# Kernel optimization log

Hardware: AMD Instinct MI355X
Metric: run time of the kernel (lower is better)

Reference implementation:

```python
import jax, jax.numpy as jnp
import numpy as np
from math import sqrt

H = 16  # head_num


def setup_inputs() -> dict:
    key = jax.random.key(0)
    ks = jax.random.split(key, 8)
    B, Sq, Skv, Dq, Dkv, Dall = 2, 2048, 2048, 1024, 1024, 1024
    x = jax.random.normal(ks[0], (B, Sq, Dq), dtype=jnp.float32)
    y = jax.random.normal(ks[1], (B, Skv, Dkv), dtype=jnp.float32)
    attention_mask = jnp.ones((B, 1, Sq, Skv), dtype=jnp.int32)
    # torch nn.Linear weights are [out, in]
    Wq = jax.random.normal(ks[2], (Dall, Dq), dtype=jnp.float32) * 0.02
    Wk = jax.random.normal(ks[3], (Dall, Dkv), dtype=jnp.float32) * 0.02
    Wv = jax.random.normal(ks[4], (Dall, Dkv), dtype=jnp.float32) * 0.02
    Wo = jax.random.normal(ks[5], (Dq, Dall), dtype=jnp.float32) * 0.02
    bo = jnp.zeros((Dq,), dtype=jnp.float32)
    return {"x": x, "y": y, "attention_mask": attention_mask,
            "Wq": Wq, "Wk": Wk, "Wv": Wv, "Wo": Wo, "bo": bo}


def reference(x, y, attention_mask, Wq, Wk, Wv, Wo, bo):
    B, Sq, _ = x.shape
    Dall = Wq.shape[0]
    Dh = Dall // H
    # projections (torch Linear: x @ W.T), split heads -> [B, H, S, Dh]
    q = (x @ Wq.T).reshape(B, Sq, H, Dh).transpose(0, 2, 1, 3)
    k = (y @ Wk.T).reshape(B, -1, H, Dh).transpose(0, 2, 1, 3)
    v = (y @ Wv.T).reshape(B, -1, H, Dh).transpose(0, 2, 1, 3)
    scores = jnp.einsum('bhqd,bhkd->bhqk', q, k)  # [B,H,Sq,Skv]
    mask = (attention_mask == 0)  # masked_fill where mask.eq(0) -> but torch does mask.eq(0) then fills True positions
    scores = jnp.where(mask, jnp.float32(-1e9), scores)
    # NOTE: faithful quirk - mask applied before scaling; scale uses sqrt(h_size)
    attn = jax.nn.softmax(scores / sqrt(Dh), axis=-1)
    out = jnp.einsum('bhqk,bhkd->bhqd', attn, v)
    out = out.transpose(0, 2, 1, 3).reshape(B, Sq, Dall)
    return out @ Wo.T + bo
```

## Files before the change

kernel.cpp:

```cpp
#include <hip/hip_runtime.h>
#include <stdint.h>


typedef __attribute__((ext_vector_type(8))) short bf16x8;
typedef __attribute__((ext_vector_type(4))) float f32x4;
typedef __attribute__((ext_vector_type(16))) float f32x16;
typedef __attribute__((ext_vector_type(2))) unsigned int u32x2;

#define LOG2E 1.44269504088896f

static __device__ __forceinline__ unsigned short f2bf(float f) {
  union { float f; unsigned int u; } v; v.f = f;
  unsigned int r = v.u + 0x7FFFu + ((v.u >> 16) & 1u);
  return (unsigned short)(r >> 16);
}

static __device__ __forceinline__ void g2l16(const void* gsrc, void* ldst) {
  __builtin_amdgcn_global_load_lds((const __attribute__((address_space(1))) unsigned int*)gsrc,
                                   (__attribute__((address_space(3))) unsigned int*)ldst,
                                   16, 0, 0);
}

static __device__ __forceinline__ unsigned int cvt_pk_bf16(float lo, float hi) {
  unsigned int r;
  asm("v_cvt_pk_bf16_f32 %0, %1, %2" : "=v"(r) : "v"(lo), "v"(hi));
  return r;
}

static __device__ __forceinline__ u32x2 pl32swap(unsigned int a, unsigned int b) {
  return __builtin_amdgcn_permlane32_swap(a, b, false, false);
}

static __device__ __forceinline__ f32x16 mfma32(bf16x8 a, bf16x8 b, f32x16 c) {
  return __builtin_amdgcn_mfma_f32_32x32x16_bf16(a, b, c, 0, 0, 0);
}

static __device__ __forceinline__ size_t kfrag_addr(int row, int col) {
  int b = row >> 11, s = row & 2047;
  int h = col >> 6, d = col & 63;
  int t32 = s >> 5, r31 = s & 31;
  int ks = d >> 4, r5 = (d >> 3) & 1, e = d & 7;
  return (size_t)(b * 16 + h) * 131072 + (size_t)t32 * 2048 + ks * 512 + (r5 * 32 + r31) * 8 + e;
}
static __device__ __forceinline__ size_t vfrag_addr(int row, int col) {
  int b = row >> 11, s = row & 2047;
  int h = col >> 6, d = col & 63;
  int t64 = s >> 6, k2 = (s >> 4) & 3, r5 = (s >> 3) & 1, e = s & 7;
  int mb = d >> 5, r31 = d & 31;
  return (size_t)(b * 16 + h) * 131072 + (size_t)t64 * 4096 + (mb * 4 + k2) * 512 + (r5 * 32 + r31) * 8 + e;
}

__global__ void k_cvt2(const float* __restrict__ a, const float* __restrict__ b,
                       unsigned short* __restrict__ oa, unsigned short* __restrict__ ob, int n) {
  const float* in = blockIdx.y ? b : a;
  unsigned short* out = blockIdx.y ? ob : oa;
  int i = (blockIdx.x * blockDim.x + threadIdx.x) * 4;
  int stride = gridDim.x * blockDim.x * 4;
  for (; i < n; i += stride) {
    float4 v = *reinterpret_cast<const float4*>(in + i);
    ushort4 o;
    o.x = f2bf(v.x); o.y = f2bf(v.y); o.z = f2bf(v.z); o.w = f2bf(v.w);
    *reinterpret_cast<ushort4*>(out + i) = o;
  }
}

__global__ void k_cvt4(const float* __restrict__ a, const float* __restrict__ b,
                       const float* __restrict__ c, const float* __restrict__ d,
                       unsigned short* __restrict__ oa, unsigned short* __restrict__ ob,
                       unsigned short* __restrict__ oc, unsigned short* __restrict__ od, int n) {
  const float* in; unsigned short* out;
  switch (blockIdx.y) {
    case 0: in = a; out = oa; break;
    case 1: in = b; out = ob; break;
    case 2: in = c; out = oc; break;
    default: in = d; out = od; break;
  }
  int i = (blockIdx.x * blockDim.x + threadIdx.x) * 4;
  int stride = gridDim.x * blockDim.x * 4;
  for (; i < n; i += stride) {
    float4 v = *reinterpret_cast<const float4*>(in + i);
    ushort4 o;
    o.x = f2bf(v.x); o.y = f2bf(v.y); o.z = f2bf(v.z); o.w = f2bf(v.w);
    *reinterpret_cast<ushort4*>(out + i) = o;
  }
}

__global__ void k_pack_mask(const int* __restrict__ mask, unsigned long long* __restrict__ bits,
                            unsigned int* __restrict__ flag) {
  size_t gw = (size_t)blockIdx.x * 4 + (threadIdx.x >> 6);
  int lane = threadIdx.x & 63;
  int m = mask[gw * 64 + lane];
  unsigned long long bal = __ballot(m != 0);
  if (lane == 0) {
    bits[gw] = bal;
    if (bal != ~0ull) atomicAnd(flag, 0u);
  }
}

template <int OM>
static __device__ __forceinline__ void gemm_body(const unsigned short* __restrict__ A,
                                                 const unsigned short* __restrict__ W,
                                                 void* __restrict__ Cout,
                                                 const float* __restrict__ bias) {
  __shared__ __align__(16) unsigned short As[128 * 32];
  __shared__ __align__(16) unsigned short Bs[128 * 32];
  const int tid = threadIdx.x;
  const int w = tid >> 6, lane = tid & 63;
  const int wr = w >> 1, wc = w & 1;
  const int l15 = lane & 15, lg = lane >> 4;
  const int bm = blockIdx.x, bn = blockIdx.y;

  f32x4 acc[4][4] = {};

  const int e0 = w * 1024 + lane * 8;
  const int e1 = e0 + 512;
  const int r0 = e0 >> 5, c0 = e0 & 31;
  const int r1 = e1 >> 5, c1 = e1 & 31;
  const unsigned short* A0 = A + (size_t)(bm * 128 + r0) * 1024 + c0;
  const unsigned short* A1 = A + (size_t)(bm * 128 + r1) * 1024 + c1;
  const unsigned short* W0 = W + (size_t)(bn * 128 + r0) * 1024 + c0;
  const unsigned short* W1 = W + (size_t)(bn * 128 + r1) * 1024 + c1;

  for (int kt = 0; kt < 1024; kt += 32) {
    g2l16(A0 + kt, (char*)As + e0 * 2);
    g2l16(A1 + kt, (char*)As + e1 * 2);
    g2l16(W0 + kt, (char*)Bs + e0 * 2);
    g2l16(W1 + kt, (char*)Bs + e1 * 2);
    __syncthreads();
    bf16x8 a[4], b[4];
#pragma unroll
    for (int mi = 0; mi < 4; ++mi)
      a[mi] = *reinterpret_cast<const bf16x8*>(As + (wr * 64 + mi * 16 + l15) * 32 + lg * 8);
#pragma unroll
    for (int ni = 0; ni < 4; ++ni)
      b[ni] = *reinterpret_cast<const bf16x8*>(Bs + (wc * 64 + ni * 16 + l15) * 32 + lg * 8);
#pragma unroll
    for (int mi = 0; mi < 4; ++mi)
#pragma unroll
      for (int ni = 0; ni < 4; ++ni)
        acc[mi][ni] = __builtin_amdgcn_mfma_f32_16x16x32_bf16(a[mi], b[ni], acc[mi][ni], 0, 0, 0);
    __syncthreads();
  }

#pragma unroll
  for (int ni = 0; ni < 4; ++ni) {
    const int gcol = bn * 128 + wc * 64 + ni * 16 + l15;
    float bv = (OM == 1) ? bias[gcol] : 0.f;
#pragma unroll
    for (int mi = 0; mi < 4; ++mi) {
#pragma unroll
      for (int r = 0; r < 4; ++r) {
        const int grow = bm * 128 + wr * 64 + mi * 16 + lg * 4 + r;
        if (OM == 0)
          ((unsigned short*)Cout)[(size_t)grow * 1024 + gcol] = f2bf(acc[mi][ni][r]);
        else if (OM == 1)
          ((float*)Cout)[(size_t)grow * 1024 + gcol] = acc[mi][ni][r] + bv;
        else if (OM == 2)
          ((unsigned short*)Cout)[kfrag_addr(grow, gcol)] = f2bf(acc[mi][ni][r]);
        else
          ((unsigned short*)Cout)[vfrag_addr(grow, gcol)] = f2bf(acc[mi][ni][r]);
      }
    }
  }
}

__global__ __launch_bounds__(256) void k_gemm_qk(
    const unsigned short* __restrict__ xb, const unsigned short* __restrict__ yb,
    const unsigned short* __restrict__ Wq, const unsigned short* __restrict__ Wk,
    unsigned short* __restrict__ Qf, unsigned short* __restrict__ Kf) {
  const int z = blockIdx.z;
  gemm_body<2>(z ? yb : xb, z ? Wk : Wq, z ? Kf : Qf, nullptr);
}

__global__ __launch_bounds__(256) void k_gemm_v(
    const unsigned short* __restrict__ yb, const unsigned short* __restrict__ Wv,
    unsigned short* __restrict__ Vf) {
  gemm_body<3>(yb, Wv, Vf, nullptr);
}

__global__ __launch_bounds__(256) void k_gemm_o(
    const unsigned short* __restrict__ AO, const unsigned short* __restrict__ Wo,
    float* __restrict__ out, const float* __restrict__ bo) {
  gemm_body<1>(AO, Wo, out, bo);
}


#define BUILD_PB2(SP, K2, IDX) {                                   \
    unsigned int c0_ = cvt_pk_bf16(SP[(K2)*8 + 0], SP[(K2)*8 + 1]);\
    unsigned int c1_ = cvt_pk_bf16(SP[(K2)*8 + 2], SP[(K2)*8 + 3]);\
    unsigned int c2_ = cvt_pk_bf16(SP[(K2)*8 + 4], SP[(K2)*8 + 5]);\
    unsigned int c3_ = cvt_pk_bf16(SP[(K2)*8 + 6], SP[(K2)*8 + 7]);\
    u32x2 r0_ = pl32swap(c0_, c2_);                                \
    u32x2 r1_ = pl32swap(c1_, c3_);                                \
    union { unsigned int u[4]; bf16x8 v; } f_;                     \
    f_.u[0] = r0_.x; f_.u[1] = r1_.x; f_.u[2] = r0_.y; f_.u[3] = r1_.y; \
    pb[IDX] = f_.v; }

#define ATTN_STEP(c0, c1, n0, n1, T)                                          \
  {                                                                           \
    const int t_ = (T);                                                       \
    _Pragma("unroll")                                                         \
    for (int f = 0; f < 8; ++f)                                               \
      vf[f] = *reinterpret_cast<const bf16x8*>(Vbase + (size_t)t_ * 4096 + f * 512); \
    n0 = z16; n1 = z16;                                                       \
    _Pragma("unroll")                                                         \
    for (int ks = 0; ks < 4; ++ks) {                                          \
      n0 = mfma32(kf[ks], qf[ks], n0);                                        \
      n1 = mfma32(kf[4 + ks], qf[ks], n1);                                    \
    }                                                                         \
    const int t2_ = (t_ + 2) & 31;                                            \
    _Pragma("unroll")                                                         \
    for (int f = 0; f < 8; ++f)                                               \
      kf[f] = *reinterpret_cast<const bf16x8*>(Kbase + (size_t)t2_ * 4096 + f * 512); \
    if (!allfull) {                                                           \
      unsigned long long wb = brow[t_];                                       \
      if (!__all(wb == ~0ull)) {                                              \
        _Pragma("unroll")                                                     \
        for (int r = 0; r < 16; ++r) {                                        \
          const int kl = (r & 3) + 8 * (r >> 2) + 4 * hi;                     \
          c0[r] = ((wb >> kl) & 1ull) ? c0[r] : -1e9f;                        \
          c1[r] = ((wb >> (kl + 32)) & 1ull) ? c1[r] : -1e9f;                 \
        }                                                                     \
      }                                                                       \
    }                                                                         \
    float mx[8];                                                              \
    _Pragma("unroll")                                                         \
    for (int r = 0; r < 8; ++r)                                               \
      mx[r] = fmaxf(fmaxf(c0[r], c0[r + 8]), fmaxf(c1[r], c1[r + 8]));        \
    mx[0] = fmaxf(mx[0], mx[4]); mx[1] = fmaxf(mx[1], mx[5]);                 \
    mx[2] = fmaxf(mx[2], mx[6]); mx[3] = fmaxf(mx[3], mx[7]);                 \
    mx[0] = fmaxf(mx[0], mx[2]); mx[1] = fmaxf(mx[1], mx[3]);                 \
    float tm = fmaxf(mx[0], mx[1]);                                           \
    {                                                                         \
      u32x2 sw = pl32swap(__builtin_bit_cast(unsigned int, tm),               \
                          __builtin_bit_cast(unsigned int, tm));              \
      tm = fmaxf(__builtin_bit_cast(float, sw.x), __builtin_bit_cast(float, sw.y)); \
    }                                                                         \
    tm *= 0.125f;                                                             \
    if (__any(tm > m_run + 8.f)) {                                            \
      const float mn = fmaxf(m_run, tm);                                      \
      const float al = __builtin_amdgcn_exp2f((m_run - mn) * LOG2E);          \
      m_run = mn; l_run *= al;                                                \
      _Pragma("unroll")                                                       \
      for (int r = 0; r < 16; ++r) { o0[r] *= al; o1[r] *= al; }              \
    }                                                                         \
    const float mc_ = m_run * LOG2E;                                          \
    _Pragma("unroll")                                                         \
    for (int r = 0; r < 16; ++r) {                                            \
      c0[r] = __builtin_amdgcn_exp2f(c0[r] * C1 - mc_);                       \
      c1[r] = __builtin_amdgcn_exp2f(c1[r] * C1 - mc_);                       \
    }                                                                         \
    float sm[8];                                                              \
    _Pragma("unroll")                                                         \
    for (int r = 0; r < 8; ++r) sm[r] = (c0[r] + c0[r + 8]) + (c1[r] + c1[r + 8]); \
    sm[0] += sm[4]; sm[1] += sm[5]; sm[2] += sm[6]; sm[3] += sm[7];           \
    sm[0] += sm[2]; sm[1] += sm[3];                                           \
    float ls = sm[0] + sm[1];                                                 \
    {                                                                         \
      u32x2 sw = pl32swap(__builtin_bit_cast(unsigned int, ls),               \
                          __builtin_bit_cast(unsigned int, ls));              \
      ls = __builtin_bit_cast(float, sw.x) + __builtin_bit_cast(float, sw.y); \
    }                                                                         \
    l_run += ls;                                                              \
    bf16x8 pb[4];                                                             \
    BUILD_PB2(c0, 0, 0) BUILD_PB2(c0, 1, 1) BUILD_PB2(c1, 0, 2) BUILD_PB2(c1, 1, 3) \
    _Pragma("unroll")                                                         \
    for (int k2 = 0; k2 < 4; ++k2) {                                          \
      o0 = mfma32(vf[k2], pb[k2], o0);                                        \
      o1 = mfma32(vf[4 + k2], pb[k2], o1);                                    \
    }                                                                         \
  }

__global__ __launch_bounds__(256, 2) void k_attn(
    const unsigned short* __restrict__ Qf, const unsigned short* __restrict__ Kf,
    const unsigned short* __restrict__ Vf, const unsigned long long* __restrict__ bits,
    const unsigned int* __restrict__ flag, unsigned short* __restrict__ AO) {
  const int tid = threadIdx.x, w = tid >> 6, lane = tid & 63;
  const int l31 = lane & 31, hi = lane >> 5;
  const int bid = blockIdx.x;
  const int xcd = bid & 7, rr = bid >> 3;
  const int j = rr & 15;
  const int g = xcd + ((rr >> 4) << 3);
  const int h = g & 15, b = g >> 4;
  const int q = j * 128 + w * 32 + l31;
  const bool allfull = (*flag == 0xFFFFFFFFu);
  const float C1 = 0.125f * LOG2E;
  const f32x16 z16 = {};

  const size_t bh = (size_t)(b * 16 + h) * 131072;
  bf16x8 qf[4];
  const unsigned short* Qp = Qf + bh + (size_t)(j * 4 + w) * 2048 + lane * 8;
#pragma unroll
  for (int ks = 0; ks < 4; ++ks)
    qf[ks] = *reinterpret_cast<const bf16x8*>(Qp + ks * 512);

  const unsigned short* Kbase = Kf + bh + lane * 8;
  const unsigned short* Vbase = Vf + bh + lane * 8;
  const unsigned long long* brow = bits + (size_t)(b * 2048 + q) * 32;

  f32x16 o0 = {}, o1 = {};
  float m_run = -3e38f, l_run = 0.f;

  bf16x8 kf[8], vf[8];
#pragma unroll
  for (int f = 0; f < 8; ++f)
    kf[f] = *reinterpret_cast<const bf16x8*>(Kbase + f * 512);
  f32x16 s0A = z16, s1A = z16, s0B = z16, s1B = z16;
#pragma unroll
  for (int ks = 0; ks < 4; ++ks) {
    s0A = mfma32(kf[ks], qf[ks], s0A);
    s1A = mfma32(kf[4 + ks], qf[ks], s1A);
  }
#pragma unroll
  for (int f = 0; f < 8; ++f)
    kf[f] = *reinterpret_cast<const bf16x8*>(Kbase + 4096 + f * 512);

  for (int tt = 0; tt < 32; tt += 2) {
    ATTN_STEP(s0A, s1A, s0B, s1B, tt)
    ATTN_STEP(s0B, s1B, s0A, s1A, tt + 1)
  }

  const float inv = 1.f / l_run;
  unsigned short* Orow = AO + (size_t)(b * 2048 + q) * 1024 + h * 64;
#pragma unroll
  for (int g2 = 0; g2 < 4; ++g2) {
    ushort4 pk;
    pk.x = f2bf(o0[g2 * 4 + 0] * inv);
    pk.y = f2bf(o0[g2 * 4 + 1] * inv);
    pk.z = f2bf(o0[g2 * 4 + 2] * inv);
    pk.w = f2bf(o0[g2 * 4 + 3] * inv);
    *reinterpret_cast<ushort4*>(Orow + 8 * g2 + 4 * hi) = pk;
    pk.x = f2bf(o1[g2 * 4 + 0] * inv);
    pk.y = f2bf(o1[g2 * 4 + 1] * inv);
    pk.z = f2bf(o1[g2 * 4 + 2] * inv);
    pk.w = f2bf(o1[g2 * 4 + 3] * inv);
    *reinterpret_cast<ushort4*>(Orow + 32 + 8 * g2 + 4 * hi) = pk;
  }
}

extern "C" void kernel_launch(void* const* d_in, const int* in_sizes, int n_in,
                              void* d_out, int out_size, void* d_ws, size_t ws_size,
                              hipStream_t stream) {
  const float* x  = (const float*)d_in[0];
  const float* y  = (const float*)d_in[1];
  const int* mask = (const int*)d_in[2];
  const float* Wq = (const float*)d_in[3];
  const float* Wk = (const float*)d_in[4];
  const float* Wv = (const float*)d_in[5];
  const float* Wo = (const float*)d_in[6];
  const float* bo = (const float*)d_in[7];

  char* ws = (char*)d_ws;
  const size_t MB = 1ull << 20;
  unsigned short* xb  = (unsigned short*)(ws + 0 * MB);
  unsigned short* yb  = (unsigned short*)(ws + 8 * MB);
  unsigned short* Wqb = (unsigned short*)(ws + 16 * MB);
  unsigned short* Wkb = (unsigned short*)(ws + 18 * MB);
  unsigned short* Wvb = (unsigned short*)(ws + 20 * MB);
  unsigned short* Wob = (unsigned short*)(ws + 22 * MB);
  unsigned short* Qf  = (unsigned short*)(ws + 24 * MB);
  unsigned short* Kf  = (unsigned short*)(ws + 32 * MB);
  unsigned short* Vf  = (unsigned short*)(ws + 40 * MB);
  unsigned short* AOb = (unsigned short*)(ws + 56 * MB);
  unsigned long long* bits = (unsigned long long*)(ws + 64 * MB);
  unsigned int* flag = (unsigned int*)(ws + 65 * MB);

  hipMemsetAsync(flag, 0xFF, 4, stream);
  k_cvt2<<<dim3(2048, 2), 256, 0, stream>>>(x, y, xb, yb, 4194304);
  k_cvt4<<<dim3(512, 4), 256, 0, stream>>>(Wq, Wk, Wv, Wo, Wqb, Wkb, Wvb, Wob, 1048576);
  k_pack_mask<<<32768, 256, 0, stream>>>(mask, bits, flag);
  k_gemm_qk<<<dim3(32, 8, 2), 256, 0, stream>>>(xb, yb, Wqb, Wkb, Qf, Kf);
  k_gemm_v<<<dim3(32, 8, 1), 256, 0, stream>>>(yb, Wvb, Vf);
  k_attn<<<512, 256, 0, stream>>>(Qf, Kf, Vf, bits, flag, AOb);
  k_gemm_o<<<dim3(32, 8, 1), 256, 0, stream>>>(AOb, Wob, (float*)d_out, bo);
}
```

Baseline: 158.7 us.

## Stage K/V tiles through double-buffered LDS in attention; merge QKV GEMM launches

The attention kernel now copies each 64-key K and V tile into shared memory with global-to-LDS loads, double-buffered, so all four waves of a block share one copy. Before, each wave read K and V straight from global memory into registers, with K software-pipelined two tiles ahead. This cuts redundant global traffic across waves but adds a __syncthreads per tile and drops the cross-tile pipelining of the QK^T MFMA. The Q/K and V projection GEMMs are also merged into one launch with grid z=3, removing one kernel launch and letting all three projections run concurrently.

```diff
diff --git a/kernel.cpp b/kernel.cpp
--- a/kernel.cpp
+++ b/kernel.cpp
@@ -164,18 +164,16 @@
   }
 }
 
-__global__ __launch_bounds__(256) void k_gemm_qk(
+__global__ __launch_bounds__(256) void k_gemm_qkv(
     const unsigned short* __restrict__ xb, const unsigned short* __restrict__ yb,
     const unsigned short* __restrict__ Wq, const unsigned short* __restrict__ Wk,
-    unsigned short* __restrict__ Qf, unsigned short* __restrict__ Kf) {
+    const unsigned short* __restrict__ Wv,
+    unsigned short* __restrict__ Qf, unsigned short* __restrict__ Kf,
+    unsigned short* __restrict__ Vf) {
   const int z = blockIdx.z;
-  gemm_body<2>(z ? yb : xb, z ? Wk : Wq, z ? Kf : Qf, nullptr);
-}
-
-__global__ __launch_bounds__(256) void k_gemm_v(
-    const unsigned short* __restrict__ yb, const unsigned short* __restrict__ Wv,
-    unsigned short* __restrict__ Vf) {
-  gemm_body<3>(yb, Wv, Vf, nullptr);
+  if (z == 0) gemm_body<2>(xb, Wq, Qf, nullptr);
+  else if (z == 1) gemm_body<2>(yb, Wk, Kf, nullptr);
+  else gemm_body<3>(yb, Wv, Vf, nullptr);
 }
 
 __global__ __launch_bounds__(256) void k_gemm_o(
@@ -196,85 +194,22 @@
     f_.u[0] = r0_.x; f_.u[1] = r1_.x; f_.u[2] = r0_.y; f_.u[3] = r1_.y; \
     pb[IDX] = f_.v; }
 
-#define ATTN_STEP(c0, c1, n0, n1, T)                                          \
-  {                                                                           \
-    const int t_ = (T);                                                       \
-    _Pragma("unroll")                                                         \
-    for (int f = 0; f < 8; ++f)                                               \
-      vf[f] = *reinterpret_cast<const bf16x8*>(Vbase + (size_t)t_ * 4096 + f * 512); \
-    n0 = z16; n1 = z16;                                                       \
-    _Pragma("unroll")                                                         \
-    for (int ks = 0; ks < 4; ++ks) {                                          \
-      n0 = mfma32(kf[ks], qf[ks], n0);                                        \
-      n1 = mfma32(kf[4 + ks], qf[ks], n1);                                    \
-    }                                                                         \
-    const int t2_ = (t_ + 2) & 31;                                            \
-    _Pragma("unroll")                                                         \
-    for (int f = 0; f < 8; ++f)                                               \
-      kf[f] = *reinterpret_cast<const bf16x8*>(Kbase + (size_t)t2_ * 4096 + f * 512); \
-    if (!allfull) {                                                           \
-      unsigned long long wb = brow[t_];                                       \
-      if (!__all(wb == ~0ull)) {                                              \
-        _Pragma("unroll")                                                     \
-        for (int r = 0; r < 16; ++r) {                                        \
-          const int kl = (r & 3) + 8 * (r >> 2) + 4 * hi;                     \
-          c0[r] = ((wb >> kl) & 1ull) ? c0[r] : -1e9f;                        \
-          c1[r] = ((wb >> (kl + 32)) & 1ull) ? c1[r] : -1e9f;                 \
-        }                                                                     \
-      }                                                                       \
-    }                                                                         \
-    float mx[8];                                                              \
-    _Pragma("unroll")                                                         \
-    for (int r = 0; r < 8; ++r)                                               \
-      mx[r] = fmaxf(fmaxf(c0[r], c0[r + 8]), fmaxf(c1[r], c1[r + 8]));        \
-    mx[0] = fmaxf(mx[0], mx[4]); mx[1] = fmaxf(mx[1], mx[5]);                 \
-    mx[2] = fmaxf(mx[2], mx[6]); mx[3] = fmaxf(mx[3], mx[7]);                 \
-    mx[0] = fmaxf(mx[0], mx[2]); mx[1] = fmaxf(mx[1], mx[3]);                 \
-    float tm = fmaxf(mx[0], mx[1]);                                           \
-    {                                                                         \
-      u32x2 sw = pl32swap(__builtin_bit_cast(unsigned int, tm),               \
-                          __builtin_bit_cast(unsigned int, tm));              \
-      tm = fmaxf(__builtin_bit_cast(float, sw.x), __builtin_bit_cast(float, sw.y)); \
-    }                                                                         \
-    tm *= 0.125f;                                                             \
-    if (__any(tm > m_run + 8.f)) {                                            \
-      const float mn = fmaxf(m_run, tm);                                      \
-      const float al = __builtin_amdgcn_exp2f((m_run - mn) * LOG2E);          \
-      m_run = mn; l_run *= al;                                                \
-      _Pragma("unroll")                                                       \
-      for (int r = 0; r < 16; ++r) { o0[r] *= al; o1[r] *= al; }              \
-    }                                                                         \
-    const float mc_ = m_run * LOG2E;                                          \
-    _Pragma("unroll")                                                         \
-    for (int r = 0; r < 16; ++r) {                                            \
-      c0[r] = __builtin_amdgcn_exp2f(c0[r] * C1 - mc_);                       \
-      c1[r] = __builtin_amdgcn_exp2f(c1[r] * C1 - mc_);                       \
-    }                                                                         \
-    float sm[8];                                                              \
-    _Pragma("unroll")                                                         \
-    for (int r = 0; r < 8; ++r) sm[r] = (c0[r] + c0[r + 8]) + (c1[r] + c1[r + 8]); \
-    sm[0] += sm[4]; sm[1] += sm[5]; sm[2] += sm[6]; sm[3] += sm[7];           \
-    sm[0] += sm[2]; sm[1] += sm[3];                                           \
-    float ls = sm[0] + sm[1];                                                 \
-    {                                                                         \
-      u32x2 sw = pl32swap(__builtin_bit_cast(unsigned int, ls),               \
-                          __builtin_bit_cast(unsigned int, ls));              \
-      ls = __builtin_bit_cast(float, sw.x) + __builtin_bit_cast(float, sw.y); \
-    }                                                                         \
-    l_run += ls;                                                              \
-    bf16x8 pb[4];                                                             \
-    BUILD_PB2(c0, 0, 0) BUILD_PB2(c0, 1, 1) BUILD_PB2(c1, 0, 2) BUILD_PB2(c1, 1, 3) \
-    _Pragma("unroll")                                                         \
-    for (int k2 = 0; k2 < 4; ++k2) {                                          \
-      o0 = mfma32(vf[k2], pb[k2], o0);                                        \
-      o1 = mfma32(vf[4 + k2], pb[k2], o1);                                    \
-    }                                                                         \
+#define STAGE_TILE(T, BUF) {                                                  \
+    const size_t toff_ = (size_t)(T) * 8192;                                  \
+    char* kb_ = smem + (BUF) * 16384;                                         \
+    const int o0_ = (w * 2 + 0) * 1024 + lane * 16;                           \
+    const int o1_ = (w * 2 + 1) * 1024 + lane * 16;                           \
+    g2l16(Kg + toff_ + o0_, kb_ + o0_);                                       \
+    g2l16(Kg + toff_ + o1_, kb_ + o1_);                                       \
+    g2l16(Vg + toff_ + o0_, kb_ + 8192 + o0_);                                \
+    g2l16(Vg + toff_ + o1_, kb_ + 8192 + o1_);                                \
   }
 
 __global__ __launch_bounds__(256, 2) void k_attn(
     const unsigned short* __restrict__ Qf, const unsigned short* __restrict__ Kf,
     const unsigned short* __restrict__ Vf, const unsigned long long* __restrict__ bits,
     const unsigned int* __restrict__ flag, unsigned short* __restrict__ AO) {
+  __shared__ __align__(16) char smem[32768];
   const int tid = threadIdx.x, w = tid >> 6, lane = tid & 63;
   const int l31 = lane & 31, hi = lane >> 5;
   const int bid = blockIdx.x;
@@ -294,30 +229,101 @@
   for (int ks = 0; ks < 4; ++ks)
     qf[ks] = *reinterpret_cast<const bf16x8*>(Qp + ks * 512);
 
-  const unsigned short* Kbase = Kf + bh + lane * 8;
-  const unsigned short* Vbase = Vf + bh + lane * 8;
+  const char* Kg = (const char*)(Kf + bh);
+  const char* Vg = (const char*)(Vf + bh);
   const unsigned long long* brow = bits + (size_t)(b * 2048 + q) * 32;
 
   f32x16 o0 = {}, o1 = {};
   float m_run = -3e38f, l_run = 0.f;
 
-  bf16x8 kf[8], vf[8];
-#pragma unroll
-  for (int f = 0; f < 8; ++f)
-    kf[f] = *reinterpret_cast<const bf16x8*>(Kbase + f * 512);
-  f32x16 s0A = z16, s1A = z16, s0B = z16, s1B = z16;
-#pragma unroll
-  for (int ks = 0; ks < 4; ++ks) {
-    s0A = mfma32(kf[ks], qf[ks], s0A);
-    s1A = mfma32(kf[4 + ks], qf[ks], s1A);
-  }
-#pragma unroll
-  for (int f = 0; f < 8; ++f)
-    kf[f] = *reinterpret_cast<const bf16x8*>(Kbase + 4096 + f * 512);
-
-  for (int tt = 0; tt < 32; tt += 2) {
-    ATTN_STEP(s0A, s1A, s0B, s1B, tt)
-    ATTN_STEP(s0B, s1B, s0A, s1A, tt + 1)
+  STAGE_TILE(0, 0)
+  __syncthreads();
+
+  for (int t = 0; t < 32; ++t) {
+    const int cur = t & 1;
+    if (t < 31) STAGE_TILE(t + 1, cur ^ 1)
+    const char* Kb = smem + cur * 16384;
+    const char* Vb = Kb + 8192;
+
+    bf16x8 kf[8], vf[8];
+#pragma unroll
+    for (int f = 0; f < 8; ++f)
+      kf[f] = *reinterpret_cast<const bf16x8*>(Kb + f * 1024 + lane * 16);
+
+    f32x16 s0 = z16, s1 = z16;
+#pragma unroll
+    for (int ks = 0; ks < 4; ++ks) {
+      s0 = mfma32(kf[ks], qf[ks], s0);
+      s1 = mfma32(kf[4 + ks], qf[ks], s1);
+    }
+
+#pragma unroll
+    for (int f = 0; f < 8; ++f)
+      vf[f] = *reinterpret_cast<const bf16x8*>(Vb + f * 1024 + lane * 16);
+
+    if (!allfull) {
+      unsigned long long wb = brow[t];
+      if (!__all(wb == ~0ull)) {
+#pragma unroll
+        for (int r = 0; r < 16; ++r) {
+          const int kl = (r & 3) + 8 * (r >> 2) + 4 * hi;
+          s0[r] = ((wb >> kl) & 1ull) ? s0[r] : -1e9f;
+          s1[r] = ((wb >> (kl + 32)) & 1ull) ? s1[r] : -1e9f;
+        }
+      }
+    }
+
+    float mx[8];
+#pragma unroll
+    for (int r = 0; r < 8; ++r)
+      mx[r] = fmaxf(fmaxf(s0[r], s0[r + 8]), fmaxf(s1[r], s1[r + 8]));
+    mx[0] = fmaxf(mx[0], mx[4]); mx[1] = fmaxf(mx[1], mx[5]);
+    mx[2] = fmaxf(mx[2], mx[6]); mx[3] = fmaxf(mx[3], mx[7]);
+    mx[0] = fmaxf(mx[0], mx[2]); mx[1] = fmaxf(mx[1], mx[3]);
+    float tm = fmaxf(mx[0], mx[1]);
+    {
+      u32x2 sw = pl32swap(__builtin_bit_cast(unsigned int, tm),
+                          __builtin_bit_cast(unsigned int, tm));
+      tm = fmaxf(__builtin_bit_cast(float, sw.x), __builtin_bit_cast(float, sw.y));
+    }
+    tm *= 0.125f;
+
+    if (__any(tm > m_run + 8.f)) {
+      const float mn = fmaxf(m_run, tm);
+      const float al = __builtin_amdgcn_exp2f((m_run - mn) * LOG2E);
+      m_run = mn; l_run *= al;
+#pragma unroll
+      for (int r = 0; r < 16; ++r) { o0[r] *= al; o1[r] *= al; }
+    }
+
+    const float mc = m_run * LOG2E;
+    float ls;
+#pragma unroll
+    for (int r = 0; r < 16; ++r) {
+      s0[r] = __builtin_amdgcn_exp2f(s0[r] * C1 - mc);
+      s1[r] = __builtin_amdgcn_exp2f(s1[r] * C1 - mc);
+    }
+    {
+      float sm[8];
+#pragma unroll
+      for (int r = 0; r < 8; ++r) sm[r] = (s0[r] + s0[r + 8]) + (s1[r] + s1[r + 8]);
+      sm[0] += sm[4]; sm[1] += sm[5]; sm[2] += sm[6]; sm[3] += sm[7];
+      sm[0] += sm[2]; sm[1] += sm[3];
+      ls = sm[0] + sm[1];
+      u32x2 sw = pl32swap(__builtin_bit_cast(unsigned int, ls),
+                          __builtin_bit_cast(unsigned int, ls));
+      ls = __builtin_bit_cast(float, sw.x) + __builtin_bit_cast(float, sw.y);
+    }
+    l_run += ls;
+
+    bf16x8 pb[4];
+    BUILD_PB2(s0, 0, 0) BUILD_PB2(s0, 1, 1) BUILD_PB2(s1, 0, 2) BUILD_PB2(s1, 1, 3)
+#pragma unroll
+    for (int k2 = 0; k2 < 4; ++k2) {
+      o0 = mfma32(vf[k2], pb[k2], o0);
+      o1 = mfma32(vf[4 + k2], pb[k2], o1);
+    }
+    __syncthreads();
   }
 
   const float inv = 1.f / l_run;
@@ -369,8 +375,7 @@
   k_cvt2<<<dim3(2048, 2), 256, 0, stream>>>(x, y, xb, yb, 4194304);
   k_cvt4<<<dim3(512, 4), 256, 0, stream>>>(Wq, Wk, Wv, Wo, Wqb, Wkb, Wvb, Wob, 1048576);
   k_pack_mask<<<32768, 256, 0, stream>>>(mask, bits, flag);
-  k_gemm_qk<<<dim3(32, 8, 2), 256, 0, stream>>>(xb, yb, Wqb, Wkb, Qf, Kf);
-  k_gemm_v<<<dim3(32, 8, 1), 256, 0, stream>>>(yb, Wvb, Vf);
+  k_gemm_qkv<<<dim3(32, 8, 3), 256, 0, stream>>>(xb, yb, Wqb, Wkb, Wvb, Qf, Kf, Vf);
   k_attn<<<512, 256, 0, stream>>>(Qf, Kf, Vf, bits, flag, AOb);
   k_gemm_o<<<dim3(32, 8, 1), 256, 0, stream>>>(AOb, Wob, (float*)d_out, bo);
 }
```

New measurement: 140.9 us. 1.13x faster.
